# Performance work log

Measured on AMD Instinct MI355X. Metric: run time of the kernel, lower is better.

The kernel has to match this reference:

```python
import jax, jax.numpy as jnp
import numpy as np

LN_EPS = 1e-5  # torch.nn.LayerNorm default


def setup_inputs() -> dict:
    key = jax.random.key(0)
    k1, k2 = jax.random.split(key)
    N, D_IN, D_OUT, G = 4096, 512, 512, 32
    x = jax.random.normal(k1, (N, D_IN), dtype=jnp.float32)
    ln_w = jnp.ones((D_IN,), dtype=jnp.float32)
    ln_b = jnp.zeros((D_IN,), dtype=jnp.float32)
    scale = 1.0 / (np.sqrt(D_IN) * np.sqrt(G))
    fouriercoeffs = jax.random.normal(k2, (2, D_OUT, D_IN, G), dtype=jnp.float32) * scale
    bias = jnp.zeros((1, D_OUT), dtype=jnp.float32)
    return {"x": x, "ln_w": ln_w, "ln_b": ln_b, "fouriercoeffs": fouriercoeffs, "bias": bias}


def reference(x, ln_w, ln_b, fouriercoeffs, bias):
    # LayerNorm over last dim
    mu = jnp.mean(x, axis=-1, keepdims=True)
    var = jnp.mean((x - mu) ** 2, axis=-1, keepdims=True)
    xn = (x - mu) * jax.lax.rsqrt(var + LN_EPS) * ln_w + ln_b
    G = fouriercoeffs.shape[-1]
    k = jnp.arange(1, G + 1, dtype=xn.dtype)           # [G]
    arg = xn[:, :, None] * k                            # [N, D_in, G]
    c = jnp.cos(arg)
    s = jnp.sin(arg)
    # contraction over (inputdim, gridsize) -> GEMM-shaped einsum
    y = jnp.einsum('big,oig->bo', c, fouriercoeffs[0])
    y = y + jnp.einsum('big,oig->bo', s, fouriercoeffs[1])
    y = y + bias
    return y
```

## Files before the change

kernel.cpp:

```cpp
#include <hip/hip_runtime.h>
#include <hip/hip_bf16.h>


#define N_ROWS 4096
#define D_IN   512
#define D_OUT  512
#define KT     16384
#define BM 256
#define BN 256
#define SPLITK 8
#define NT 64

typedef short short8 __attribute__((ext_vector_type(8)));
typedef float float4v __attribute__((ext_vector_type(4)));

__device__ inline unsigned int pack2bf(float a, float b) {
    __hip_bfloat162 h = __float22bfloat162_rn(make_float2(a, b));
    union { __hip_bfloat162 h; unsigned int u; } cv;
    cv.h = h;
    return cv.u;
}

__device__ inline unsigned short bf16_1(float a) {
    union { float f; unsigned int u; } cv;
    cv.f = a;
    unsigned int r = (cv.u + 0x7fff + ((cv.u >> 16) & 1)) >> 16;
    return (unsigned short)r;
}

__global__ __launch_bounds__(256) void pre_kernel(const float* __restrict__ x,
        const float* __restrict__ lnw, const float* __restrict__ lnb,
        const float* __restrict__ fc, float2* __restrict__ csT,
        unsigned short* __restrict__ Wb) {
    __shared__ __align__(16) float xs[16 * 516];
    __shared__ float2 murs[16];
    const int t = threadIdx.x;
    const int r0 = blockIdx.x * 16;
    {
        const int row = t >> 4, tq = t & 15;
        const float* xr = x + (size_t)(r0 + row) * D_IN;
        float s = 0.f, q = 0.f;
        #pragma unroll
        for (int k = 0; k < 8; ++k) {
            float4 v = *(const float4*)(xr + tq * 4 + k * 64);
            *(float4*)&xs[row * 516 + tq * 4 + k * 64] = v;
            s += v.x + v.y + v.z + v.w;
            q += v.x * v.x + v.y * v.y + v.z * v.z + v.w * v.w;
        }
        #pragma unroll
        for (int off = 8; off > 0; off >>= 1) {
            s += __shfl_xor(s, off, 16);
            q += __shfl_xor(q, off, 16);
        }
        if (tq == 0) {
            float mu = s * (1.f / D_IN);
            float var = q * (1.f / D_IN) - mu * mu;
            murs[row] = make_float2(mu, rsqrtf(var + 1e-5f));
        }
    }
    __syncthreads();
    {
        const int brow = t & 15, dimg = t >> 4;
        const float2 mr = murs[brow];
        #pragma unroll 4
        for (int j = 0; j < 32; ++j) {
            const int dim = j * 16 + dimg;
            float xv = xs[brow * 516 + dim];
            float xn = (xv - mr.x) * mr.y * lnw[dim] + lnb[dim];
            float s1, c1;
            __sincosf(xn, &s1, &c1);
            csT[(size_t)dim * N_ROWS + r0 + brow] = make_float2(c1, s1);
        }
    }
    {
        size_t e = ((size_t)blockIdx.x * 256 + t) * 8;
        for (int it2 = 0; it2 < 32; ++it2, e += (size_t)256 * 256 * 8) {
            const float4* in = (const float4*)(fc + e);
            float4 a = in[0], c = in[1];
            uint4 o;
            o.x = pack2bf(a.x, a.y);
            o.y = pack2bf(a.z, a.w);
            o.z = pack2bf(c.x, c.y);
            o.w = pack2bf(c.z, c.w);
            *(uint4*)(Wb + e) = o;
        }
    }
}

__device__ inline void stage_feats(unsigned short* Abuf, float2 cs, int ttype,
                                   int frow, int ihalf) {
    const float c1 = cs.x, s1 = cs.y;
    const float c2 = c1 + c1;
    float prev = ttype ? 0.f : 1.f;
    float cur  = ttype ? s1 : c1;
    const int rbase = frow * 64;
    const int sw = frow & 7;
    unsigned int us[4];
    #pragma unroll
    for (int d = 0; d < 16; ++d) {
        float f0 = cur;
        float f1 = __builtin_fmaf(c2, cur, -prev);
        float f2 = __builtin_fmaf(c2, f1, -cur);
        prev = f1;
        cur = f2;
        us[d & 3] = pack2bf(f0, f1);
        if ((d & 3) == 3) {
            const int kc = ihalf * 4 + (d >> 2);
            *(uint4*)&Abuf[rbase + ((kc ^ sw) << 3)] =
                make_uint4(us[0], us[1], us[2], us[3]);
        }
    }
}

__device__ inline void gl_lds16(const unsigned short* gsrc, unsigned short* ldst) {
    __builtin_amdgcn_global_load_lds(
        (const __attribute__((address_space(1))) unsigned int*)gsrc,
        (__attribute__((address_space(3))) unsigned int*)ldst, 16, 0, 0);
}

template<bool PF>
__device__ __forceinline__ void gemm_tile(int tt,
        const unsigned short* Ap, const unsigned short* Bp,
        unsigned short* Aw, unsigned short* Bw,
        const unsigned short* Bg0, const float2* csBase, float2& csA,
        int wv, int wrow, int lm, int lq, int swA, int bBase,
        int arow, int adim, float4v (&acc)[8][4]) {
    const int ttype1 = ((tt + 1) >> 5) & 1;
    const float c2 = csA.x + csA.x;
    float prev = ttype1 ? 0.f : 1.f;
    float cur  = ttype1 ? csA.y : csA.x;
    float2 csN = csA;
    short8 bf[2][4];
    #pragma unroll
    for (int p = 0; p < 4; ++p) {
        short8 af[2][2];
        #pragma unroll
        for (int h = 0; h < 2; ++h)
            #pragma unroll
            for (int j = 0; j < 2; ++j)
                af[h][j] = *(const short8*)
                    &Ap[(wrow * 128 + (2 * p + j) * 16 + lm) * 64
                        + (((h * 4 + lq) ^ swA) << 3)];
        if (p == 0) {
            #pragma unroll
            for (int h = 0; h < 2; ++h)
                #pragma unroll
                for (int n = 0; n < 4; ++n)
                    bf[h][n] = *(const short8*)&Bp[bBase + n * 1024 + h * 256];
            if (PF) {
                const int n1 = tt + 1;
                const unsigned short* gb =
                    Bg0 + (size_t)(n1 >> 5) * D_OUT * KT + (n1 & 31) * 64;
                unsigned short* ldst = Bw + (wv * 4) * 512;
                #pragma unroll
                for (int j2 = 0; j2 < 4; ++j2)
                    gl_lds16(gb + (size_t)(j2 * 8) * KT, ldst + j2 * 512);
                __builtin_amdgcn_sched_barrier(0);
                csN = csBase[(size_t)(((tt + 2) & 31) * 2) * N_ROWS];
            }
        }
        if (PF) {
            unsigned int us[4];
            #pragma unroll
            for (int d = 0; d < 4; ++d) {
                float f0 = cur;
                float f1 = __builtin_fmaf(c2, cur, -prev);
                us[d] = pack2bf(f0, f1);
                float f2 = __builtin_fmaf(c2, f1, -cur);
                prev = f1;
                cur = f2;
            }
            const int kc = adim * 4 + p;
            *(uint4*)&Aw[arow * 64 + ((kc ^ (arow & 7)) << 3)] =
                make_uint4(us[0], us[1], us[2], us[3]);
        }
        __builtin_amdgcn_s_barrier();
        asm volatile("s_waitcnt lgkmcnt(0)" ::: "memory");
        __builtin_amdgcn_s_setprio(1);
        #pragma unroll
        for (int h = 0; h < 2; ++h)
            #pragma unroll
            for (int j = 0; j < 2; ++j)
                #pragma unroll
                for (int n = 0; n < 4; ++n)
                    acc[2 * p + j][n] = __builtin_amdgcn_mfma_f32_16x16x32_bf16(
                        af[h][j], bf[h][n], acc[2 * p + j][n], 0, 0, 0);
        __builtin_amdgcn_s_setprio(0);
        if (p < 3) {
            __builtin_amdgcn_s_barrier();
            asm volatile("" ::: "memory");
        } else if (PF) {
            asm volatile("s_waitcnt vmcnt(1)" ::: "memory");
            __builtin_amdgcn_s_barrier();
            asm volatile("" ::: "memory");
        }
    }
    if (PF) csA = csN;
}

__global__ __launch_bounds__(512, 2) void fkan_gemm(const float2* __restrict__ csT,
        const unsigned short* __restrict__ Wb, unsigned short* __restrict__ pb) {
    __shared__ unsigned short As[2][BM * 64];
    __shared__ unsigned short Bs[2][BN * 64];
    const int t = threadIdx.x;
    const int row0 = blockIdx.x * BM;
    const int col0 = blockIdx.y * BN;
    const int kz = blockIdx.z;
    const int k0 = kz * 2048;
    const int i0 = kz * 64;
    const int l = t & 63, wv = t >> 6;
    const int wrow = wv >> 2, wcol = wv & 3;
    const int lm = l & 15, lq = l >> 4;
    const int swA = lm & 7;
    const int arow = t & 255, adim = t >> 8;
    const int c8 = l & 7, s8 = l >> 3;
    const unsigned short* Bg0 =
        Wb + (size_t)(col0 + wv * 32 + c8) * KT + k0 + s8 * 8;
    const int bBase = (wcol * 8 + (lm >> 3)) * 512 + lq * 64 + (lm & 7) * 8;
    const float2* csBase = csT + (size_t)(i0 + adim) * N_ROWS + row0 + arow;

    float4v acc[8][4];
    #pragma unroll
    for (int i = 0; i < 8; ++i)
        #pragma unroll
        for (int j = 0; j < 4; ++j)
            acc[i][j] = (float4v){0.f, 0.f, 0.f, 0.f};

    float2 cs0 = csBase[0];
    #pragma unroll
    for (int j = 0; j < 4; ++j)
        gl_lds16(Bg0 + (size_t)(j * 8) * KT, &Bs[0][(wv * 4 + j) * 512]);
    __builtin_amdgcn_sched_barrier(0);
    float2 csA = csBase[2 * N_ROWS];
    stage_feats(&As[0][0], cs0, 0, arow, adim);
    asm volatile("s_waitcnt vmcnt(1) lgkmcnt(0)" ::: "memory");
    __builtin_amdgcn_s_barrier();
    asm volatile("" ::: "memory");

    #pragma unroll 1
    for (int tt = 0; tt < NT - 1; ++tt)
        gemm_tile<true>(tt, &As[tt & 1][0], &Bs[tt & 1][0],
                        &As[(tt + 1) & 1][0], &Bs[(tt + 1) & 1][0],
                        Bg0, csBase, csA, wv, wrow, lm, lq, swA, bBase,
                        arow, adim, acc);
    gemm_tile<false>(NT - 1, &As[1][0], &Bs[1][0], &As[0][0], &Bs[0][0],
                     Bg0, csBase, csA, wv, wrow, lm, lq, swA, bBase,
                     arow, adim, acc);

    unsigned short* pc = pb + (size_t)kz * N_ROWS * D_OUT;
    #pragma unroll
    for (int m = 0; m < 8; ++m)
        #pragma unroll
        for (int n = 0; n < 4; ++n)
            #pragma unroll
            for (int r = 0; r < 4; ++r) {
                const int row = row0 + wrow * 128 + m * 16 + lq * 4 + r;
                const int col = col0 + wcol * 64 + n * 16 + lm;
                pc[(size_t)row * D_OUT + col] = bf16_1(acc[m][n][r]);
            }
}

__global__ __launch_bounds__(256) void reduce_kernel(const unsigned short* __restrict__ pb,
        const float* __restrict__ bias, float* __restrict__ out) {
    const size_t e = ((size_t)blockIdx.x * 256 + threadIdx.x) * 4;
    const int col = (int)(e & (D_OUT - 1));
    float4 s = *(const float4*)(bias + col);
    #pragma unroll
    for (int c = 0; c < SPLITK; ++c) {
        ushort4 u = *(const ushort4*)(pb + (size_t)c * N_ROWS * D_OUT + e);
        union { unsigned int u; float f; } f0, f1, f2, f3;
        f0.u = (unsigned int)u.x << 16;
        f1.u = (unsigned int)u.y << 16;
        f2.u = (unsigned int)u.z << 16;
        f3.u = (unsigned int)u.w << 16;
        s.x += f0.f; s.y += f1.f; s.z += f2.f; s.w += f3.f;
    }
    *(float4*)(out + e) = s;
}

extern "C" void kernel_launch(void* const* d_in, const int* in_sizes, int n_in,
                              void* d_out, int out_size, void* d_ws, size_t ws_size,
                              hipStream_t stream) {
    const float* x    = (const float*)d_in[0];
    const float* ln_w = (const float*)d_in[1];
    const float* ln_b = (const float*)d_in[2];
    const float* fc   = (const float*)d_in[3];
    const float* bias = (const float*)d_in[4];
    float* out = (float*)d_out;

    float2* csT = (float2*)d_ws;
    unsigned short* Wb = (unsigned short*)((char*)d_ws + (16u << 20));
    unsigned short* pbp = (unsigned short*)((char*)d_ws + (48u << 20));

    pre_kernel<<<256, 256, 0, stream>>>(x, ln_w, ln_b, fc, csT, Wb);
    fkan_gemm<<<dim3(N_ROWS / BM, D_OUT / BN, SPLITK), 512, 0, stream>>>(csT, Wb, pbp);
    reduce_kernel<<<2048, 256, 0, stream>>>(pbp, bias, out);
}
```

Before: 253.6 us.

## Reorder GEMM inner loop by k-half and widen reduce kernel loads

Result: no change. 256.9 us (+1.3%).

```diff
diff --git a/kernel.cpp b/kernel.cpp
--- a/kernel.cpp
+++ b/kernel.cpp
@@ -130,35 +130,42 @@
     float prev = ttype1 ? 0.f : 1.f;
     float cur  = ttype1 ? csA.y : csA.x;
     float2 csN = csA;
-    short8 bf[2][4];
+    short8 bf[4];
     #pragma unroll
     for (int p = 0; p < 4; ++p) {
-        short8 af[2][2];
-        #pragma unroll
-        for (int h = 0; h < 2; ++h)
-            #pragma unroll
-            for (int j = 0; j < 2; ++j)
-                af[h][j] = *(const short8*)
-                    &Ap[(wrow * 128 + (2 * p + j) * 16 + lm) * 64
-                        + (((h * 4 + lq) ^ swA) << 3)];
-        if (p == 0) {
-            #pragma unroll
-            for (int h = 0; h < 2; ++h)
-                #pragma unroll
-                for (int n = 0; n < 4; ++n)
-                    bf[h][n] = *(const short8*)&Bp[bBase + n * 1024 + h * 256];
-            if (PF) {
-                const int n1 = tt + 1;
-                const unsigned short* gb =
-                    Bg0 + (size_t)(n1 >> 5) * D_OUT * KT + (n1 & 31) * 64;
-                unsigned short* ldst = Bw + (wv * 4) * 512;
-                #pragma unroll
-                for (int j2 = 0; j2 < 4; ++j2)
-                    gl_lds16(gb + (size_t)(j2 * 8) * KT, ldst + j2 * 512);
-                __builtin_amdgcn_sched_barrier(0);
-                csN = csBase[(size_t)(((tt + 2) & 31) * 2) * N_ROWS];
-            }
-        }
+        const int mh = p & 1, h = p >> 1;
+        short8 af[4];
+        #pragma unroll
+        for (int j = 0; j < 4; ++j)
+            af[j] = *(const short8*)
+                &Ap[(wrow * 128 + (4 * mh + j) * 16 + lm) * 64
+                    + (((h * 4 + lq) ^ swA) << 3)];
+        if (p == 0 || p == 2) {
+            #pragma unroll
+            for (int n = 0; n < 4; ++n)
+                bf[n] = *(const short8*)&Bp[bBase + n * 1024 + h * 256];
+        }
+        if (PF && p == 0) {
+            const int n1 = tt + 1;
+            const unsigned short* gb =
+                Bg0 + (size_t)(n1 >> 5) * D_OUT * KT + (n1 & 31) * 64;
+            unsigned short* ldst = Bw + (wv * 4) * 512;
+            #pragma unroll
+            for (int j2 = 0; j2 < 4; ++j2)
+                gl_lds16(gb + (size_t)(j2 * 8) * KT, ldst + j2 * 512);
+            __builtin_amdgcn_sched_barrier(0);
+            csN = csBase[(size_t)(((tt + 2) & 31) * 2) * N_ROWS];
+        }
+        __builtin_amdgcn_s_barrier();
+        asm volatile("s_waitcnt lgkmcnt(0)" ::: "memory");
+        __builtin_amdgcn_s_setprio(1);
+        #pragma unroll
+        for (int j = 0; j < 4; ++j)
+            #pragma unroll
+            for (int n = 0; n < 4; ++n)
+                acc[4 * mh + j][n] = __builtin_amdgcn_mfma_f32_16x16x32_bf16(
+                    af[j], bf[n], acc[4 * mh + j][n], 0, 0, 0);
+        __builtin_amdgcn_s_setprio(0);
         if (PF) {
             unsigned int us[4];
             #pragma unroll
@@ -174,23 +181,11 @@
             *(uint4*)&Aw[arow * 64 + ((kc ^ (arow & 7)) << 3)] =
                 make_uint4(us[0], us[1], us[2], us[3]);
         }
-        __builtin_amdgcn_s_barrier();
-        asm volatile("s_waitcnt lgkmcnt(0)" ::: "memory");
-        __builtin_amdgcn_s_setprio(1);
-        #pragma unroll
-        for (int h = 0; h < 2; ++h)
-            #pragma unroll
-            for (int j = 0; j < 2; ++j)
-                #pragma unroll
-                for (int n = 0; n < 4; ++n)
-                    acc[2 * p + j][n] = __builtin_amdgcn_mfma_f32_16x16x32_bf16(
-                        af[h][j], bf[h][n], acc[2 * p + j][n], 0, 0, 0);
-        __builtin_amdgcn_s_setprio(0);
         if (p < 3) {
             __builtin_amdgcn_s_barrier();
             asm volatile("" ::: "memory");
         } else if (PF) {
-            asm volatile("s_waitcnt vmcnt(1)" ::: "memory");
+            asm volatile("s_waitcnt vmcnt(1) lgkmcnt(0)" ::: "memory");
             __builtin_amdgcn_s_barrier();
             asm volatile("" ::: "memory");
         }
@@ -262,20 +257,25 @@
 
 __global__ __launch_bounds__(256) void reduce_kernel(const unsigned short* __restrict__ pb,
         const float* __restrict__ bias, float* __restrict__ out) {
-    const size_t e = ((size_t)blockIdx.x * 256 + threadIdx.x) * 4;
+    const size_t e = ((size_t)blockIdx.x * 256 + threadIdx.x) * 8;
     const int col = (int)(e & (D_OUT - 1));
-    float4 s = *(const float4*)(bias + col);
+    float4 s0 = *(const float4*)(bias + col);
+    float4 s1 = *(const float4*)(bias + col + 4);
     #pragma unroll
     for (int c = 0; c < SPLITK; ++c) {
-        ushort4 u = *(const ushort4*)(pb + (size_t)c * N_ROWS * D_OUT + e);
-        union { unsigned int u; float f; } f0, f1, f2, f3;
-        f0.u = (unsigned int)u.x << 16;
-        f1.u = (unsigned int)u.y << 16;
-        f2.u = (unsigned int)u.z << 16;
-        f3.u = (unsigned int)u.w << 16;
-        s.x += f0.f; s.y += f1.f; s.z += f2.f; s.w += f3.f;
-    }
-    *(float4*)(out + e) = s;
+        uint4 u = *(const uint4*)(pb + (size_t)c * N_ROWS * D_OUT + e);
+        union { unsigned int u; float f; } lo, hi;
+        lo.u = u.x << 16;            hi.u = u.x & 0xffff0000u;
+        s0.x += lo.f;                s0.y += hi.f;
+        lo.u = u.y << 16;            hi.u = u.y & 0xffff0000u;
+        s0.z += lo.f;                s0.w += hi.f;
+        lo.u = u.z << 16;            hi.u = u.z & 0xffff0000u;
+        s1.x += lo.f;                s1.y += hi.f;
+        lo.u = u.w << 16;            hi.u = u.w & 0xffff0000u;
+        s1.z += lo.f;                s1.w += hi.f;
+    }
+    *(float4*)(out + e) = s0;
+    *(float4*)(out + e + 4) = s1;
 }
 
 extern "C" void kernel_launch(void* const* d_in, const int* in_sizes, int n_in,
@@ -294,5 +294,5 @@
 
     pre_kernel<<<256, 256, 0, stream>>>(x, ln_w, ln_b, fc, csT, Wb);
     fkan_gemm<<<dim3(N_ROWS / BM, D_OUT / BN, SPLITK), 512, 0, stream>>>(csT, Wb, pbp);
-    reduce_kernel<<<2048, 256, 0, stream>>>(pbp, bias, out);
-}
+    reduce_kernel<<<1024, 256, 0, stream>>>(pbp, bias, out);
+}
```
